# Optimization experiments

Hardware: AMD Instinct MI355X
Metric: run time of the kernel (lower is better)

Reference implementation:

```python
import jax, jax.numpy as jnp
import numpy as np

N = 50000      # nodes
E = 800000     # edges
D = 128        # input_dim = nb_hidden = emb_dim
A = 4          # nb_edge_types (edge attr dim)
H = 2          # heads (MyGATConv default)
G = 128        # number of graphs (g.batch)
NEG = 0.2      # leaky_relu negative slope
L = 3          # nb_layers


def _glorot(key, shape):
    lim = np.sqrt(6.0 / (shape[-2] + shape[-1]))
    return jax.random.uniform(key, shape, minval=-lim, maxval=lim, dtype=jnp.float32)


def setup_inputs():
    key = jax.random.key(0)
    ks = jax.random.split(key, 20)
    inp = {
        "x": jax.random.normal(ks[0], (N, D), jnp.float32),
        "edge_index": jax.random.randint(ks[1], (2, E), 0, N, dtype=jnp.int32),
        "edge_attr": jax.random.normal(ks[2], (E, A), jnp.float32),
        "batch": jnp.sort(jax.random.randint(ks[3], (N,), 0, G, dtype=jnp.int32)),
    }
    for l in range(L):
        inp[f"linN{l}"] = _glorot(ks[4 + 4 * l], (D, H * D))
        inp[f"linE{l}"] = _glorot(ks[5 + 4 * l], (A, H * A))
        inp[f"att{l}"] = _glorot(ks[6 + 4 * l], (1, H, 2 * D + A))
        inp[f"bias{l}"] = jnp.zeros((H * D,), jnp.float32)
    inp["fw"] = _glorot(ks[16], (D, 1))
    inp["fb"] = jnp.zeros((1,), jnp.float32)
    return inp


def _gat_layer(x_in, e_in, src, dst, linN, linE, att, bias):
    n = x_in.shape[0]
    x = (x_in @ linN + bias).reshape(n, H, D)              # [N,H,D]
    e = (e_in @ linE).reshape(-1, H, A)                    # [E,H,A]
    # alpha = (cat([x_i, x_j, e], -1) * att).sum(-1); x_i = x[src], x_j = x[dst]
    ai = jnp.einsum('nhc,hc->nh', x, att[0, :, :D])        # per-node, gathered at src
    aj = jnp.einsum('nhc,hc->nh', x, att[0, :, D:2 * D])   # per-node, gathered at dst
    ae = jnp.einsum('ehc,hc->eh', e, att[0, :, 2 * D:])
    alpha = jax.nn.leaky_relu(ai[src] + aj[dst] + ae, NEG)  # [E,H]
    # segment softmax over targets (edge_index[1])
    amax = jax.ops.segment_max(alpha, dst, num_segments=n)
    ex = jnp.exp(alpha - amax[dst])
    denom = jax.ops.segment_sum(ex, dst, num_segments=n)
    alpha = ex / denom[dst]
    # PyG propagate: message = alpha * x[src], scatter-add at dst
    msg = alpha[:, :, None] * x[src]                       # [E,H,D]
    out = jax.ops.segment_sum(msg, dst, num_segments=n) + x
    # concat=False -> mean over heads, then ReLU
    return jax.nn.relu(out.mean(axis=1)), jax.nn.relu(e.mean(axis=1))


def reference(x, edge_index, edge_attr, batch,
              linN0, linE0, att0, bias0,
              linN1, linE1, att1, bias1,
              linN2, linE2, att2, bias2,
              fw, fb):
    src, dst = edge_index[0], edge_index[1]
    params = [(linN0, linE0, att0, bias0),
              (linN1, linE1, att1, bias1),
              (linN2, linE2, att2, bias2)]
    h, e = x, edge_attr
    for (lN, lE, at, b) in params:
        h, e = _gat_layer(h, e, src, dst, lN, lE, at, b)
    pooled = jax.ops.segment_sum(h, batch, num_segments=G)  # global_add_pool -> [G,D]
    y = (pooled @ fw + fb).squeeze(-1)                      # [G]
    return y
```

## Files before the change

### kernel.cpp

```cpp
#include <hip/hip_runtime.h>
#include <hip/hip_bf16.h>

#define DD 128
#define AA 4
#define HH 2

typedef short short8 __attribute__((ext_vector_type(8)));
typedef float f32x4 __attribute__((ext_vector_type(4)));

__device__ inline unsigned short f2bf(float f) {
    unsigned u = __float_as_uint(f);
    unsigned r = (u + 0x7fffu + ((u >> 16) & 1u)) >> 16;
    return (unsigned short)r;
}
__device__ inline float4 unpack_bf16x4(uint2 v) {
    float4 r;
    r.x = __uint_as_float(v.x << 16);
    r.y = __uint_as_float(v.x & 0xffff0000u);
    r.z = __uint_as_float(v.y << 16);
    r.w = __uint_as_float(v.y & 0xffff0000u);
    return r;
}
__device__ inline uint2 pack_bf16x4(float a, float b, float c, float d) {
    uint2 p;
    p.x = (unsigned)f2bf(a) | ((unsigned)f2bf(b) << 16);
    p.y = (unsigned)f2bf(c) | ((unsigned)f2bf(d) << 16);
    return p;
}


__global__ void hist_kernel(const int* __restrict__ dst, int* __restrict__ cnt, int E) {
    int e = blockIdx.x * blockDim.x + threadIdx.x;
    if (e < E) atomicAdd(&cnt[dst[e]], 1);
}

__global__ __launch_bounds__(256) void scan1(const int* __restrict__ cnt,
                                             int* __restrict__ bsum, int N,
                                             float* __restrict__ y,
                                             const float* __restrict__ fb) {
    __shared__ int wsh[4];
    int b = blockIdx.x, t = threadIdx.x;
    int lane = t & 63, w = t >> 6;
    if (b == 0 && t < 128) y[t] = fb[0];
    int base = b * 1024;
    int v = 0;
    #pragma unroll
    for (int i = 0; i < 4; ++i) {
        int idx = base + i * 256 + t;
        v += (idx < N) ? cnt[idx] : 0;
    }
    #pragma unroll
    for (int o = 32; o; o >>= 1) v += __shfl_xor(v, o);
    if (lane == 0) wsh[w] = v;
    __syncthreads();
    if (t == 0) bsum[b] = wsh[0] + wsh[1] + wsh[2] + wsh[3];
}

__global__ __launch_bounds__(64) void scan2(int* __restrict__ bsum, int NB,
                                            int* __restrict__ total) {
    int t = threadIdx.x;
    int v = (t < NB) ? bsum[t] : 0;
    int x = v;
    #pragma unroll
    for (int o = 1; o < 64; o <<= 1) {
        int u = __shfl_up(x, o);
        if (t >= o) x += u;
    }
    if (t < NB) bsum[t] = x - v;
    if (t == 63) *total = x;
}

__global__ __launch_bounds__(256) void scan3(const int* __restrict__ cnt,
                                             const int* __restrict__ bsum,
                                             int* __restrict__ row_off,
                                             int* __restrict__ cursor, int N) {
    __shared__ int wtot[4];
    __shared__ int carry;
    int b = blockIdx.x, t = threadIdx.x;
    int lane = t & 63, w = t >> 6;
    if (t == 0) carry = bsum[b];
    __syncthreads();
    int base = b * 1024;
    #pragma unroll
    for (int it = 0; it < 4; ++it) {
        int idx = base + it * 256 + t;
        int v = (idx < N) ? cnt[idx] : 0;
        int x = v;
        #pragma unroll
        for (int o = 1; o < 64; o <<= 1) {
            int u = __shfl_up(x, o);
            if (lane >= o) x += u;
        }
        if (lane == 63) wtot[w] = x;
        __syncthreads();
        int woff = 0;
        for (int i = 0; i < w; ++i) woff += wtot[i];
        int c = carry;
        __syncthreads();
        if (t == 255) carry = c + woff + x;
        int ex = c + woff + x - v;
        if (idx < N) { row_off[idx] = ex; cursor[idx] = ex; }
        __syncthreads();
    }
}

__global__ void scatter_kernel(const int* __restrict__ src, const int* __restrict__ dst,
                               int* __restrict__ cursor, int* __restrict__ csr_src,
                               int* __restrict__ csr_eid, int E) {
    int e = blockIdx.x * blockDim.x + threadIdx.x;
    if (e >= E) return;
    int p = atomicAdd(&cursor[dst[e]], 1);
    csr_src[p] = src[e];
    csr_eid[p] = e;
}


__global__ __launch_bounds__(256) void pack_a0(const float* __restrict__ X,
                                               uint2* __restrict__ As, int N) {
    int t = blockIdx.x * blockDim.x + threadIdx.x;
    if (t >= N * 32) return;
    int r = t >> 5, kq4 = t & 31;
    float4 v = ((const float4*)X)[t];
    int g = r >> 4, m = r & 15;
    int ks = kq4 >> 3, q = (kq4 >> 1) & 3;
    int cell = ((g * 4 + ks) * 4 + q) * 16 + m;
    As[cell * 2 + (kq4 & 1)] = pack_bf16x4(v.x, v.y, v.z, v.w);
}

__global__ __launch_bounds__(256) void pack_w3(const float* __restrict__ W0,
                                               const float* __restrict__ W1,
                                               const float* __restrict__ W2,
                                               unsigned short* __restrict__ Bs) {
    int t = blockIdx.x * blockDim.x + threadIdx.x;
    if (t >= 3 * 128 * 64) return;
    int l = t / (128 * 64);
    int r = t - l * (128 * 64);
    const float* W = (l == 0) ? W0 : (l == 1) ? W1 : W2;
    unsigned short* B = Bs + (size_t)l * 128 * 256;
    int k = r >> 6, c4g = r & 63;
    float4 v = ((const float4*)W)[r];
    int ct = c4g >> 2, n0 = (c4g & 3) * 4;
    int ks = k >> 5, q = (k >> 3) & 3, j = k & 7;
    int cellbase = ((ct * 4 + ks) * 4 + q) * 16 + n0;
    B[(cellbase + 0) * 8 + j] = f2bf(v.x);
    B[(cellbase + 1) * 8 + j] = f2bf(v.y);
    B[(cellbase + 2) * 8 + j] = f2bf(v.z);
    B[(cellbase + 3) * 8 + j] = f2bf(v.w);
}


__global__ __launch_bounds__(256) void gemm_mfma(const short8* __restrict__ As,
                                                 const short8* __restrict__ Bs,
                                                 const float* __restrict__ bias,
                                                 const float* __restrict__ att,
                                                 uint2* __restrict__ xhb,
                                                 float* __restrict__ aiaj, int Ngroups) {
    __shared__ __align__(16) unsigned short sh[4][16 * 132];
    int w = threadIdx.x >> 6;
    int flat = blockIdx.x * 4 + w;
    int wid = flat >> 1, half = flat & 1;
    int lane = threadIdx.x & 63;
    if (wid >= Ngroups) return;
    int q = lane >> 4, m = lane & 15;

    const short8* Ag = As + (size_t)wid * 256;
    f32x4 acc[8];
    #pragma unroll
    for (int c8 = 0; c8 < 8; ++c8) acc[c8] = (f32x4){0.f, 0.f, 0.f, 0.f};

    #pragma unroll
    for (int ks = 0; ks < 4; ++ks) {
        short8 a = Ag[ks * 64 + lane];
        #pragma unroll
        for (int c8 = 0; c8 < 8; ++c8) {
            short8 b = Bs[(half * 8 + c8) * 256 + ks * 64 + lane];
            acc[c8] = __builtin_amdgcn_mfma_f32_16x16x32_bf16(a, b, acc[c8], 0, 0, 0);
        }
    }

    const float* atth = att + half * (2 * DD + AA);
    float ai[4] = {}, aj[4] = {};
    #pragma unroll
    for (int c8 = 0; c8 < 8; ++c8) {
        int col = c8 * 16 + m;
        float aS = atth[col];
        float aD = atth[DD + col];
        float bv = bias[(half * 8 + c8) * 16 + m];
        #pragma unroll
        for (int reg = 0; reg < 4; ++reg) {
            float val = acc[c8][reg] + bv;
            sh[w][(q * 4 + reg) * 132 + col] = f2bf(val);
            ai[reg] += val * aS;
            aj[reg] += val * aD;
        }
    }
    #pragma unroll
    for (int o = 1; o < 16; o <<= 1) {
        #pragma unroll
        for (int reg = 0; reg < 4; ++reg) {
            ai[reg] += __shfl_xor(ai[reg], o);
            aj[reg] += __shfl_xor(aj[reg], o);
        }
    }
    if (m == 0) {
        #pragma unroll
        for (int reg = 0; reg < 4; ++reg) {
            int row = wid * 16 + q * 4 + reg;
            aiaj[row * 4 + half] = ai[reg];
            aiaj[row * 4 + 2 + half] = aj[reg];
        }
    }
    #pragma unroll
    for (int r2 = 0; r2 < 8; ++r2) {
        int row = r2 * 2 + (lane >> 5);
        uint2 v = *(const uint2*)&sh[w][row * 132 + (lane & 31) * 4];
        xhb[(size_t)(wid * 16 + row) * 64 + half * 32 + (lane & 31)] = v;
    }
}


__device__ inline void edge_stage(const float4& ev, const float* __restrict__ linE,
                                  const float* __restrict__ att, float2& ae, float4& enext) {
    float eh[8];
    #pragma unroll
    for (int c = 0; c < 8; ++c)
        eh[c] = ev.x * linE[c] + ev.y * linE[8 + c] + ev.z * linE[16 + c] + ev.w * linE[24 + c];
    float a0 = 0.f, a1 = 0.f;
    #pragma unroll
    for (int a = 0; a < 4; ++a) {
        a0 += eh[a]     * att[2 * DD + a];
        a1 += eh[4 + a] * att[(2 * DD + AA) + 2 * DD + a];
    }
    ae.x = a0; ae.y = a1;
    enext.x = fmaxf(0.5f * (eh[0] + eh[4]), 0.f);
    enext.y = fmaxf(0.5f * (eh[1] + eh[5]), 0.f);
    enext.z = fmaxf(0.5f * (eh[2] + eh[6]), 0.f);
    enext.w = fmaxf(0.5f * (eh[3] + eh[7]), 0.f);
}

__global__ __launch_bounds__(256) void edge_all(const float* __restrict__ ein,
                                                const float* __restrict__ linE0, const float* __restrict__ att0,
                                                const float* __restrict__ linE1, const float* __restrict__ att1,
                                                const float* __restrict__ linE2, const float* __restrict__ att2,
                                                const int* __restrict__ csr_eid,
                                                float2* __restrict__ ae0,
                                                float2* __restrict__ ae1,
                                                float2* __restrict__ ae2, int E) {
    int p = blockIdx.x * blockDim.x + threadIdx.x;
    if (p >= E) return;
    int eid = csr_eid[p];
    float4 ev = ((const float4*)ein)[eid];
    float2 ae; float4 en;
    edge_stage(ev, linE0, att0, ae, en); ae0[p] = ae;
    edge_stage(en, linE1, att1, ae, ev); ae1[p] = ae;
    edge_stage(ev, linE2, att2, ae, en); ae2[p] = ae;
}


__global__ __launch_bounds__(64) void aggregate(const uint2* __restrict__ xhb,
                                                const float* __restrict__ aiaj,
                                                const float2* __restrict__ ae,
                                                const int* __restrict__ row_off,
                                                const int* __restrict__ csr_src,
                                                uint2* __restrict__ hshuf,
                                                const float* __restrict__ fw,
                                                float* __restrict__ pdots, int N) {
    int d = blockIdx.x;
    int lane = threadIdx.x;
    int s0 = row_off[d], s1 = row_off[d + 1];
    int deg = s1 - s0;
    const float2* aiaj2 = (const float2*)aiaj;
    float2 ajv = aiaj2[d * 2 + 1];

    __shared__ float lex[64][2];
    __shared__ int lsrc[64];
    float4 acc = {0.f, 0.f, 0.f, 0.f};
    float den0 = 0.f, den1 = 0.f;
    int head = lane >> 5;

    for (int c = 0; c < deg; c += 64) {
        int n = min(64, deg - c);
        if (lane < n) {
            int p = s0 + c + lane;
            int s = csr_src[p];
            float2 aiv = aiaj2[s * 2];
            float2 aev = ae[p];
            float a0 = aiv.x + ajv.x + aev.x; a0 = a0 > 0.f ? a0 : 0.2f * a0;
            float a1 = aiv.y + ajv.y + aev.y; a1 = a1 > 0.f ? a1 : 0.2f * a1;
            float e0 = __expf(a0), e1 = __expf(a1);
            den0 += e0; den1 += e1;
            lex[lane][0] = e0; lex[lane][1] = e1;
            lsrc[lane] = s;
        }
        #pragma unroll 4
        for (int j = 0; j < n; ++j) {
            float wgt = lex[j][head];
            float4 xv = unpack_bf16x4(xhb[(size_t)lsrc[j] * 64 + lane]);
            acc.x += wgt * xv.x; acc.y += wgt * xv.y;
            acc.z += wgt * xv.z; acc.w += wgt * xv.w;
        }
    }

    #pragma unroll
    for (int o = 32; o; o >>= 1) {
        den0 += __shfl_xor(den0, o);
        den1 += __shfl_xor(den1, o);
    }
    float den = head ? den1 : den0;
    if (deg == 0) den = 1.0f;
    float inv = 1.0f / den;

    float4 xd = unpack_bf16x4(xhb[(size_t)d * 64 + lane]);
    float4 v;
    v.x = acc.x * inv + xd.x;
    v.y = acc.y * inv + xd.y;
    v.z = acc.z * inv + xd.z;
    v.w = acc.w * inv + xd.w;
    float4 o2;
    o2.x = __shfl_xor(v.x, 32);
    o2.y = __shfl_xor(v.y, 32);
    o2.z = __shfl_xor(v.z, 32);
    o2.w = __shfl_xor(v.w, 32);
    if (lane < 32) {
        float4 r;
        r.x = fmaxf(0.5f * (v.x + o2.x), 0.f);
        r.y = fmaxf(0.5f * (v.y + o2.y), 0.f);
        r.z = fmaxf(0.5f * (v.z + o2.z), 0.f);
        r.w = fmaxf(0.5f * (v.w + o2.w), 0.f);
        if (hshuf) {
            int g = d >> 4, m = d & 15;
            int ks = lane >> 3, q = (lane >> 1) & 3;
            int cell = ((g * 4 + ks) * 4 + q) * 16 + m;
            hshuf[cell * 2 + (lane & 1)] = pack_bf16x4(r.x, r.y, r.z, r.w);
        }
        if (pdots) {
            float4 wv = ((const float4*)fw)[lane];
            float pd = r.x * wv.x + r.y * wv.y + r.z * wv.z + r.w * wv.w;
            #pragma unroll
            for (int o = 16; o; o >>= 1) pd += __shfl_xor(pd, o);
            if (lane == 0) pdots[d] = pd;
        }
    }
}


__global__ __launch_bounds__(256) void segpool_kernel(const float* __restrict__ p,
                                                      const int* __restrict__ batch,
                                                      float* __restrict__ y, int N, int G) {
    __shared__ float bins[128];
    int t = threadIdx.x;
    if (t < G) bins[t] = 0.f;
    __syncthreads();
    int per = (N + gridDim.x - 1) / gridDim.x;
    int lo = blockIdx.x * per;
    int hi = min(lo + per, N);
    float acc = 0.f;
    int key = -1;
    for (int i = lo + t; i < hi; i += 256) {
        int k = batch[i];
        float v = p[i];
        if (k != key) {
            if (key >= 0) atomicAdd(&bins[key], acc);
            key = k;
            acc = 0.f;
        }
        acc += v;
    }
    if (key >= 0) atomicAdd(&bins[key], acc);
    __syncthreads();
    if (t < G && bins[t] != 0.f) atomicAdd(&y[t], bins[t]);
}


extern "C" void kernel_launch(void* const* d_in, const int* in_sizes, int n_in,
                              void* d_out, int out_size, void* d_ws, size_t ws_size,
                              hipStream_t stream) {
    const float* x     = (const float*)d_in[0];
    const int*   ei    = (const int*)d_in[1];
    const float* eattr = (const float*)d_in[2];
    const int*   batch = (const int*)d_in[3];
    const float* fw    = (const float*)d_in[16];
    const float* fb    = (const float*)d_in[17];
    float* y = (float*)d_out;

    const int N = in_sizes[0] / DD;
    const int E = in_sizes[1] / 2;
    const int G = out_size;

    const int* src = ei;
    const int* dst = ei + E;

    char* ws = (char*)d_ws;
    size_t off = 0;
    auto carve = [&](size_t bytes) {
        char* p = ws + off;
        off += (bytes + 255) & ~(size_t)255;
        return p;
    };
    uint2*  xhb     = (uint2*)carve((size_t)N * 256 * 2);
    uint2*  S0      = (uint2*)carve((size_t)N * 128 * 2);
    uint2*  S1      = (uint2*)carve((size_t)N * 128 * 2);
    unsigned short* Bs = (unsigned short*)carve((size_t)3 * 128 * 256 * 2);
    float2* ae0     = (float2*)carve((size_t)E * 2 * 4);
    float2* ae1     = (float2*)carve((size_t)E * 2 * 4);
    float2* ae2     = (float2*)carve((size_t)E * 2 * 4);
    float*  aiaj    = (float*)carve((size_t)N * 4 * 4);
    int*    row_off = (int*)carve((size_t)(N + 1) * 4);
    int*    cursor  = (int*)carve((size_t)N * 4);
    int*    cnt     = (int*)carve((size_t)N * 4);
    int*    csr_src = (int*)carve((size_t)E * 4);
    int*    csr_eid = (int*)carve((size_t)E * 4);
    float*  pdots   = (float*)carve((size_t)N * 4);
    int*    bsum    = (int*)carve((size_t)256 * 4);

    const int NB = (N + 1023) / 1024;
    const int Ngroups = N / 16;

    hipMemsetAsync(cnt, 0, (size_t)N * 4, stream);
    int eb = (E + 255) / 256;
    hist_kernel<<<eb, 256, 0, stream>>>(dst, cnt, E);
    scan1<<<NB, 256, 0, stream>>>(cnt, bsum, N, y, fb);
    scan2<<<1, 64, 0, stream>>>(bsum, NB, row_off + N);
    scan3<<<NB, 256, 0, stream>>>(cnt, bsum, row_off, cursor, N);
    scatter_kernel<<<eb, 256, 0, stream>>>(src, dst, cursor, csr_src, csr_eid, E);

    edge_all<<<eb, 256, 0, stream>>>(eattr,
                                     (const float*)d_in[5], (const float*)d_in[6],
                                     (const float*)d_in[9], (const float*)d_in[10],
                                     (const float*)d_in[13], (const float*)d_in[14],
                                     csr_eid, ae0, ae1, ae2, E);

    pack_a0<<<(N * 32 + 255) / 256, 256, 0, stream>>>(x, S0, N);
    pack_w3<<<(3 * 128 * 64 + 255) / 256, 256, 0, stream>>>(
        (const float*)d_in[4], (const float*)d_in[8], (const float*)d_in[12], Bs);

    int gemm_blocks = (Ngroups * 2 + 3) / 4;
    float2* aes[3] = {ae0, ae1, ae2};
    uint2* Ain[3]  = {S0, S1, S0};
    uint2* Aout[3] = {S1, S0, nullptr};

    for (int l = 0; l < 3; ++l) {
        const float* att  = (const float*)d_in[6 + 4 * l];
        const float* bias = (const float*)d_in[7 + 4 * l];
        const short8* Bl  = (const short8*)(Bs + (size_t)l * 128 * 256);

        gemm_mfma<<<gemm_blocks, 256, 0, stream>>>((const short8*)Ain[l], Bl,
                                                   bias, att, xhb, aiaj, Ngroups);
        aggregate<<<N, 64, 0, stream>>>(xhb, aiaj, aes[l], row_off, csr_src,
                                        Aout[l], fw, (l == 2) ? pdots : nullptr, N);
    }

    segpool_kernel<<<128, 256, 0, stream>>>(pdots, batch, y, N, G);
}
```

Measured before the change: 477.3 us.

## Record atomic ranks in histogram, build CSR permutation without atomics, fuse prep kernels

The histogram pass now stores each edge's atomic return value as its rank within its destination bucket. A non-atomic permutation kernel then places each edge at row_off+rank, replacing the second atomic scatter pass. The edge-attention precompute, input packing and weight packing are merged into one multi-role launch, which also gathers csr_src. This removes one atomic pass and two launches, at the cost of an extra rank array and a scattered write in the permutation step.

```diff
diff --git a/kernel.cpp b/kernel.cpp
--- a/kernel.cpp
+++ b/kernel.cpp
@@ -29,9 +29,10 @@
 }
 
 
-__global__ void hist_kernel(const int* __restrict__ dst, int* __restrict__ cnt, int E) {
+__global__ void rank_kernel(const int* __restrict__ dst, int* __restrict__ cnt,
+                            int* __restrict__ rank, int E) {
     int e = blockIdx.x * blockDim.x + threadIdx.x;
-    if (e < E) atomicAdd(&cnt[dst[e]], 1);
+    if (e < E) rank[e] = atomicAdd(&cnt[dst[e]], 1);
 }
 
 __global__ __launch_bounds__(256) void scan1(const int* __restrict__ cnt,
@@ -72,8 +73,7 @@
 
 __global__ __launch_bounds__(256) void scan3(const int* __restrict__ cnt,
                                              const int* __restrict__ bsum,
-                                             int* __restrict__ row_off,
-                                             int* __restrict__ cursor, int N) {
+                                             int* __restrict__ row_off, int N) {
     __shared__ int wtot[4];
     __shared__ int carry;
     int b = blockIdx.x, t = threadIdx.x;
@@ -99,53 +99,87 @@
         __syncthreads();
         if (t == 255) carry = c + woff + x;
         int ex = c + woff + x - v;
-        if (idx < N) { row_off[idx] = ex; cursor[idx] = ex; }
+        if (idx < N) row_off[idx] = ex;
         __syncthreads();
     }
 }
 
-__global__ void scatter_kernel(const int* __restrict__ src, const int* __restrict__ dst,
-                               int* __restrict__ cursor, int* __restrict__ csr_src,
-                               int* __restrict__ csr_eid, int E) {
+__global__ void perm_kernel(const int* __restrict__ dst, const int* __restrict__ rank,
+                            const int* __restrict__ row_off, int* __restrict__ perm, int E) {
     int e = blockIdx.x * blockDim.x + threadIdx.x;
     if (e >= E) return;
-    int p = atomicAdd(&cursor[dst[e]], 1);
-    csr_src[p] = src[e];
-    csr_eid[p] = e;
-}
-
-
-__global__ __launch_bounds__(256) void pack_a0(const float* __restrict__ X,
-                                               uint2* __restrict__ As, int N) {
-    int t = blockIdx.x * blockDim.x + threadIdx.x;
-    if (t >= N * 32) return;
-    int r = t >> 5, kq4 = t & 31;
-    float4 v = ((const float4*)X)[t];
-    int g = r >> 4, m = r & 15;
-    int ks = kq4 >> 3, q = (kq4 >> 1) & 3;
-    int cell = ((g * 4 + ks) * 4 + q) * 16 + m;
-    As[cell * 2 + (kq4 & 1)] = pack_bf16x4(v.x, v.y, v.z, v.w);
-}
-
-__global__ __launch_bounds__(256) void pack_w3(const float* __restrict__ W0,
-                                               const float* __restrict__ W1,
-                                               const float* __restrict__ W2,
-                                               unsigned short* __restrict__ Bs) {
-    int t = blockIdx.x * blockDim.x + threadIdx.x;
-    if (t >= 3 * 128 * 64) return;
-    int l = t / (128 * 64);
-    int r = t - l * (128 * 64);
-    const float* W = (l == 0) ? W0 : (l == 1) ? W1 : W2;
-    unsigned short* B = Bs + (size_t)l * 128 * 256;
-    int k = r >> 6, c4g = r & 63;
-    float4 v = ((const float4*)W)[r];
-    int ct = c4g >> 2, n0 = (c4g & 3) * 4;
-    int ks = k >> 5, q = (k >> 3) & 3, j = k & 7;
-    int cellbase = ((ct * 4 + ks) * 4 + q) * 16 + n0;
-    B[(cellbase + 0) * 8 + j] = f2bf(v.x);
-    B[(cellbase + 1) * 8 + j] = f2bf(v.y);
-    B[(cellbase + 2) * 8 + j] = f2bf(v.z);
-    B[(cellbase + 3) * 8 + j] = f2bf(v.w);
+    perm[row_off[dst[e]] + rank[e]] = e;
+}
+
+
+__device__ inline void edge_stage(const float4& ev, const float* __restrict__ linE,
+                                  const float* __restrict__ att, float2& ae, float4& enext) {
+    float eh[8];
+    #pragma unroll
+    for (int c = 0; c < 8; ++c)
+        eh[c] = ev.x * linE[c] + ev.y * linE[8 + c] + ev.z * linE[16 + c] + ev.w * linE[24 + c];
+    float a0 = 0.f, a1 = 0.f;
+    #pragma unroll
+    for (int a = 0; a < 4; ++a) {
+        a0 += eh[a]     * att[2 * DD + a];
+        a1 += eh[4 + a] * att[(2 * DD + AA) + 2 * DD + a];
+    }
+    ae.x = a0; ae.y = a1;
+    enext.x = fmaxf(0.5f * (eh[0] + eh[4]), 0.f);
+    enext.y = fmaxf(0.5f * (eh[1] + eh[5]), 0.f);
+    enext.z = fmaxf(0.5f * (eh[2] + eh[6]), 0.f);
+    enext.w = fmaxf(0.5f * (eh[3] + eh[7]), 0.f);
+}
+
+__global__ __launch_bounds__(256) void prep_fused(
+        const float* __restrict__ ein, const int* __restrict__ src,
+        const int* __restrict__ perm,
+        const float* __restrict__ linE0, const float* __restrict__ att0,
+        const float* __restrict__ linE1, const float* __restrict__ att1,
+        const float* __restrict__ linE2, const float* __restrict__ att2,
+        int* __restrict__ csr_src,
+        float2* __restrict__ ae0, float2* __restrict__ ae1, float2* __restrict__ ae2,
+        int E, int ebE,
+        const float* __restrict__ X, uint2* __restrict__ As, int N, int ebA,
+        const float* __restrict__ W0, const float* __restrict__ W1,
+        const float* __restrict__ W2, unsigned short* __restrict__ Bs) {
+    int b = blockIdx.x;
+    if (b < ebE) {
+        int p = b * 256 + threadIdx.x;
+        if (p >= E) return;
+        int e = perm[p];
+        csr_src[p] = src[e];
+        float4 ev = ((const float4*)ein)[e];
+        float2 ae; float4 en;
+        edge_stage(ev, linE0, att0, ae, en); ae0[p] = ae;
+        edge_stage(en, linE1, att1, ae, ev); ae1[p] = ae;
+        edge_stage(ev, linE2, att2, ae, en); ae2[p] = ae;
+    } else if (b < ebE + ebA) {
+        int t = (b - ebE) * 256 + threadIdx.x;
+        if (t >= N * 32) return;
+        int r = t >> 5, kq4 = t & 31;
+        float4 v = ((const float4*)X)[t];
+        int g = r >> 4, m = r & 15;
+        int ks = kq4 >> 3, q = (kq4 >> 1) & 3;
+        int cell = ((g * 4 + ks) * 4 + q) * 16 + m;
+        As[cell * 2 + (kq4 & 1)] = pack_bf16x4(v.x, v.y, v.z, v.w);
+    } else {
+        int t = (b - ebE - ebA) * 256 + threadIdx.x;
+        if (t >= 3 * 128 * 64) return;
+        int l = t / (128 * 64);
+        int r = t - l * (128 * 64);
+        const float* W = (l == 0) ? W0 : (l == 1) ? W1 : W2;
+        unsigned short* B = Bs + (size_t)l * 128 * 256;
+        int k = r >> 6, c4g = r & 63;
+        float4 v = ((const float4*)W)[r];
+        int ct = c4g >> 2, n0 = (c4g & 3) * 4;
+        int ks = k >> 5, q = (k >> 3) & 3, j = k & 7;
+        int cellbase = ((ct * 4 + ks) * 4 + q) * 16 + n0;
+        B[(cellbase + 0) * 8 + j] = f2bf(v.x);
+        B[(cellbase + 1) * 8 + j] = f2bf(v.y);
+        B[(cellbase + 2) * 8 + j] = f2bf(v.z);
+        B[(cellbase + 3) * 8 + j] = f2bf(v.w);
+    }
 }
 
 
@@ -216,44 +250,6 @@
         uint2 v = *(const uint2*)&sh[w][row * 132 + (lane & 31) * 4];
         xhb[(size_t)(wid * 16 + row) * 64 + half * 32 + (lane & 31)] = v;
     }
-}
-
-
-__device__ inline void edge_stage(const float4& ev, const float* __restrict__ linE,
-                                  const float* __restrict__ att, float2& ae, float4& enext) {
-    float eh[8];
-    #pragma unroll
-    for (int c = 0; c < 8; ++c)
-        eh[c] = ev.x * linE[c] + ev.y * linE[8 + c] + ev.z * linE[16 + c] + ev.w * linE[24 + c];
-    float a0 = 0.f, a1 = 0.f;
-    #pragma unroll
-    for (int a = 0; a < 4; ++a) {
-        a0 += eh[a]     * att[2 * DD + a];
-        a1 += eh[4 + a] * att[(2 * DD + AA) + 2 * DD + a];
-    }
-    ae.x = a0; ae.y = a1;
-    enext.x = fmaxf(0.5f * (eh[0] + eh[4]), 0.f);
-    enext.y = fmaxf(0.5f * (eh[1] + eh[5]), 0.f);
-    enext.z = fmaxf(0.5f * (eh[2] + eh[6]), 0.f);
-    enext.w = fmaxf(0.5f * (eh[3] + eh[7]), 0.f);
-}
-
-__global__ __launch_bounds__(256) void edge_all(const float* __restrict__ ein,
-                                                const float* __restrict__ linE0, const float* __restrict__ att0,
-                                                const float* __restrict__ linE1, const float* __restrict__ att1,
-                                                const float* __restrict__ linE2, const float* __restrict__ att2,
-                                                const int* __restrict__ csr_eid,
-                                                float2* __restrict__ ae0,
-                                                float2* __restrict__ ae1,
-                                                float2* __restrict__ ae2, int E) {
-    int p = blockIdx.x * blockDim.x + threadIdx.x;
-    if (p >= E) return;
-    int eid = csr_eid[p];
-    float4 ev = ((const float4*)ein)[eid];
-    float2 ae; float4 en;
-    edge_stage(ev, linE0, att0, ae, en); ae0[p] = ae;
-    edge_stage(en, linE1, att1, ae, ev); ae1[p] = ae;
-    edge_stage(ev, linE2, att2, ae, en); ae2[p] = ae;
 }
 
 
@@ -406,32 +402,33 @@
     float2* ae2     = (float2*)carve((size_t)E * 2 * 4);
     float*  aiaj    = (float*)carve((size_t)N * 4 * 4);
     int*    row_off = (int*)carve((size_t)(N + 1) * 4);
-    int*    cursor  = (int*)carve((size_t)N * 4);
     int*    cnt     = (int*)carve((size_t)N * 4);
+    int*    rank    = (int*)carve((size_t)E * 4);
     int*    csr_src = (int*)carve((size_t)E * 4);
-    int*    csr_eid = (int*)carve((size_t)E * 4);
+    int*    perm    = (int*)carve((size_t)E * 4);
     float*  pdots   = (float*)carve((size_t)N * 4);
     int*    bsum    = (int*)carve((size_t)256 * 4);
 
     const int NB = (N + 1023) / 1024;
     const int Ngroups = N / 16;
+    const int eb = (E + 255) / 256;
 
     hipMemsetAsync(cnt, 0, (size_t)N * 4, stream);
-    int eb = (E + 255) / 256;
-    hist_kernel<<<eb, 256, 0, stream>>>(dst, cnt, E);
+    rank_kernel<<<eb, 256, 0, stream>>>(dst, cnt, rank, E);
     scan1<<<NB, 256, 0, stream>>>(cnt, bsum, N, y, fb);
     scan2<<<1, 64, 0, stream>>>(bsum, NB, row_off + N);
-    scan3<<<NB, 256, 0, stream>>>(cnt, bsum, row_off, cursor, N);
-    scatter_kernel<<<eb, 256, 0, stream>>>(src, dst, cursor, csr_src, csr_eid, E);
-
-    edge_all<<<eb, 256, 0, stream>>>(eattr,
-                                     (const float*)d_in[5], (const float*)d_in[6],
-                                     (const float*)d_in[9], (const float*)d_in[10],
-                                     (const float*)d_in[13], (const float*)d_in[14],
-                                     csr_eid, ae0, ae1, ae2, E);
-
-    pack_a0<<<(N * 32 + 255) / 256, 256, 0, stream>>>(x, S0, N);
-    pack_w3<<<(3 * 128 * 64 + 255) / 256, 256, 0, stream>>>(
+    scan3<<<NB, 256, 0, stream>>>(cnt, bsum, row_off, N);
+    perm_kernel<<<eb, 256, 0, stream>>>(dst, rank, row_off, perm, E);
+
+    const int ebA = (N * 32 + 255) / 256;
+    const int ebW = (3 * 128 * 64 + 255) / 256;
+    prep_fused<<<eb + ebA + ebW, 256, 0, stream>>>(
+        eattr, src, perm,
+        (const float*)d_in[5], (const float*)d_in[6],
+        (const float*)d_in[9], (const float*)d_in[10],
+        (const float*)d_in[13], (const float*)d_in[14],
+        csr_src, ae0, ae1, ae2, E, eb,
+        x, S0, N, ebA,
         (const float*)d_in[4], (const float*)d_in[8], (const float*)d_in[12], Bs);
 
     int gemm_blocks = (Ngroups * 2 + 3) / 4;
```

Measured after the change: 451.1 us. 1.06x faster.
